# Performance work log

Hardware: AMD Instinct MI355X
Metric: run time of the kernel (lower is better)

## Reference

```python
import jax, jax.numpy as jnp
import numpy as np

B, T, C = 4, 2048, 1024
H = 16
D = C // H  # head_dim = 64

def setup_inputs() -> dict:
    key = jax.random.key(0)
    ks = jax.random.split(key, 5)
    scale = 0.02
    x = jax.random.normal(ks[0], (B, T, C), dtype=jnp.float32)
    # weights stored [in, out] (transpose of torch Linear layout; same math)
    Wqkv = jax.random.normal(ks[1], (C, 3 * C), dtype=jnp.float32) * scale
    bqkv = jnp.zeros((3 * C,), dtype=jnp.float32)
    Wproj = jax.random.normal(ks[2], (C, C), dtype=jnp.float32) * scale
    bproj = jnp.zeros((C,), dtype=jnp.float32)
    return {"x": x, "Wqkv": Wqkv, "bqkv": bqkv, "Wproj": Wproj, "bproj": bproj}

def reference(x, Wqkv, bqkv, Wproj, bproj):
    Bx, Tx, Cx = x.shape
    qkv = x @ Wqkv + bqkv                      # [B,T,3C]
    q, k, v = jnp.split(qkv, 3, axis=2)
    # [B,T,C] -> [B,H,T,D]
    q = q.reshape(Bx, Tx, H, D).transpose(0, 2, 1, 3)
    k = k.reshape(Bx, Tx, H, D).transpose(0, 2, 1, 3)
    v = v.reshape(Bx, Tx, H, D).transpose(0, 2, 1, 3)
    att = jnp.einsum('bhqd,bhkd->bhqk', q, k) / jnp.sqrt(jnp.float32(D))
    causal = jnp.tril(jnp.ones((Tx, Tx), dtype=bool))
    att = jnp.where(causal, att, jnp.float32(-jnp.inf))
    att = jax.nn.softmax(att, axis=-1)
    y = jnp.einsum('bhqk,bhkd->bhqd', att, v)  # [B,H,T,D]
    y = y.transpose(0, 2, 1, 3).reshape(Bx, Tx, Cx)
    return y @ Wproj + bproj
```

## Files before the change

### kernel.cpp

```cpp
#include <hip/hip_runtime.h>
#include <math.h>

#define Bb 4
#define Tt 2048
#define Cc 1024
#define Hh 16
#define Dd 64
#define QSC 0.18033688011112042f

typedef unsigned short ushort_t;
typedef __attribute__((ext_vector_type(8))) short short8;
typedef __attribute__((ext_vector_type(4))) float floatx4;

typedef unsigned int __attribute__((address_space(1))) u32_as1;
typedef unsigned int __attribute__((address_space(3))) u32_as3;

__device__ __forceinline__ void gld_lds16(const void* g, const void* lds_uniform) {
    __builtin_amdgcn_global_load_lds(
        (const u32_as1*)(unsigned long long)g,
        (u32_as3*)(unsigned int)(unsigned long long)lds_uniform,
        16, 0, 0);
}

__device__ inline ushort_t f2bf(float x) {
    unsigned int u = __float_as_uint(x);
    return (ushort_t)((u + 0x7FFFu + ((u >> 16) & 1u)) >> 16);
}

__device__ __forceinline__ void bar() {
    asm volatile("" ::: "memory");
    __builtin_amdgcn_s_barrier();
    asm volatile("" ::: "memory");
}

__global__ __launch_bounds__(256) void convert_kernel(
    const float* __restrict__ in, ushort_t* __restrict__ out, int n4)
{
    int i = blockIdx.x * 256 + threadIdx.x;
    if (i < n4) {
        float4 v = *(const float4*)&in[i * 4];
        ushort_t o[4] = {f2bf(v.x), f2bf(v.y), f2bf(v.z), f2bf(v.w)};
        *(uint2*)&out[i * 4] = *(uint2*)o;
    }
}

__global__ __launch_bounds__(256) void transpose_kernel(
    const float* __restrict__ W, ushort_t* __restrict__ Wt, int K, int N)
{
    __shared__ ushort_t Ts[16][72];
    const int n0 = blockIdx.x * 64;
    const int k0 = blockIdx.y * 16;
    const int t = threadIdx.x;
#pragma unroll
    for (int i = 0; i < 4; i++) {
        int e = t + i * 256;
        int kl = e >> 6, nl = e & 63;
        Ts[kl][nl] = f2bf(W[(size_t)(k0 + kl) * N + n0 + nl]);
    }
    __syncthreads();
    {
        int nl = t >> 2, kl4 = (t & 3) * 4;
        ushort_t o[4] = {Ts[kl4][nl], Ts[kl4 + 1][nl], Ts[kl4 + 2][nl], Ts[kl4 + 3][nl]};
        *(uint2*)&Wt[(size_t)(n0 + nl) * K + k0 + kl4] = *(uint2*)o;
    }
}

template <bool OUT_BF16, bool SCALE_Q>
__global__ __launch_bounds__(512) void gemm256_kernel(
    const ushort_t* __restrict__ A, const ushort_t* __restrict__ Bt,
    const float* __restrict__ bias, void* __restrict__ Co,
    int M, int N, int K)
{
    __shared__ __align__(16) ushort_t Ls[65536];

    const int tid = threadIdx.x;
    const int lane = tid & 63;
    const int w = tid >> 6;
    const int wm = w >> 2, wn = w & 3;
    const int l = lane & 15, q = lane >> 4;
    const int NT = K >> 6;

    const int n0 = blockIdx.x * 256;
    const int m0 = blockIdx.y * 256;

    const int ln = lane ^ (((lane >> 5) & 1) << 1);
    const ushort_t* Ag = A  + (size_t)(m0 + w * 16 + (ln >> 2)) * K + (ln & 3) * 8;
    const ushort_t* Bg = Bt + (size_t)(n0 + w * 16 + (ln >> 2)) * K + (ln & 3) * 8;

    const int swz = l * 32 + ((q * 8) ^ (((l >> 3) & 1) << 4));

    floatx4 acc[2][2][4][2];
#pragma unroll
    for (int qm = 0; qm < 2; qm++)
#pragma unroll
        for (int qn = 0; qn < 2; qn++)
#pragma unroll
            for (int mf = 0; mf < 4; mf++)
#pragma unroll
                for (int nf = 0; nf < 2; nf++)
                    acc[qm][qn][mf][nf] = (floatx4){0.f, 0.f, 0.f, 0.f};

    short8 af[4][2], bf0[2][2], bf1[2][2];

#define STAGE_(SLOT, MAT, HALF, T, GB) {                                        \
    const ushort_t* _g = (GB) + (size_t)(HALF) * 128 * K + (size_t)(T) * 64;    \
    const ushort_t* _l = &Ls[(SLOT) * 32768 + (MAT) * 16384 + (HALF) * 8192 + w * 1024]; \
    gld_lds16(_g, _l);                                                          \
    gld_lds16(_g + 32, _l + 512); }
#define STAGE_A(SLOT, HALF, T) STAGE_((SLOT), 0, (HALF), (T), Ag)
#define STAGE_B(SLOT, HALF, T) STAGE_((SLOT), 1, (HALF), (T), Bg)

#define LDA(SLOT, QM) {                                                         \
    _Pragma("unroll") for (int mf = 0; mf < 4; mf++)                            \
    _Pragma("unroll") for (int kc = 0; kc < 2; kc++)                            \
        af[mf][kc] = *(const short8*)&Ls[(SLOT) * 32768 + (QM) * 8192 +         \
            ((wm * 4 + mf) * 2 + kc) * 512 + swz]; }

#define LDB(SLOT, QN, DST) {                                                    \
    _Pragma("unroll") for (int nf = 0; nf < 2; nf++)                            \
    _Pragma("unroll") for (int kc = 0; kc < 2; kc++)                            \
        DST[nf][kc] = *(const short8*)&Ls[(SLOT) * 32768 + 16384 + (QN) * 8192 + \
            ((wn * 2 + nf) * 2 + kc) * 512 + swz]; }

#define MM(QM, QN, BF) {                                                        \
    __builtin_amdgcn_s_setprio(1);                                              \
    _Pragma("unroll") for (int kc = 0; kc < 2; kc++)                            \
    _Pragma("unroll") for (int mf = 0; mf < 4; mf++)                            \
    _Pragma("unroll") for (int nf = 0; nf < 2; nf++)                            \
        acc[QM][QN][mf][nf] = __builtin_amdgcn_mfma_f32_16x16x32_bf16(          \
            af[mf][kc], BF[nf][kc], acc[QM][QN][mf][nf], 0, 0, 0);              \
    __builtin_amdgcn_s_setprio(0); }

#define LGKM0() asm volatile("s_waitcnt lgkmcnt(0)" ::: "memory")

    STAGE_A(0, 0, 0); STAGE_B(0, 0, 0); STAGE_B(0, 1, 0); STAGE_A(0, 1, 0);
    if (NT > 1) {
        STAGE_A(1, 0, 1); STAGE_B(1, 0, 1); STAGE_B(1, 1, 1);
        asm volatile("s_waitcnt vmcnt(6)" ::: "memory");
    } else {
        asm volatile("s_waitcnt vmcnt(0)" ::: "memory");
    }
    bar();

    for (int g = 0; g < NT; ++g) {
        const int slot = g & 1;

        LDA(slot, 0);
        LDB(slot, 0, bf0);
        if (g + 1 < NT) STAGE_A(slot ^ 1, 1, g + 1);
        bar();
        LGKM0();
        MM(0, 0, bf0);
        bar();

        LDB(slot, 1, bf1);
        if (g + 2 < NT) STAGE_A(slot, 0, g + 2);
        bar();
        LGKM0();
        MM(0, 1, bf1);
        bar();

        LDA(slot, 1);
        if (g + 2 < NT) STAGE_B(slot, 0, g + 2);
        bar();
        LGKM0();
        MM(1, 1, bf1);
        bar();

        if (g + 2 < NT) STAGE_B(slot, 1, g + 2);
        bar();
        LGKM0();
        MM(1, 0, bf0);
        if (g + 1 < NT) {
            if (g + 2 < NT) asm volatile("s_waitcnt vmcnt(6)" ::: "memory");
            else            asm volatile("s_waitcnt vmcnt(0)" ::: "memory");
            bar();
        }
    }

#pragma unroll
    for (int qn = 0; qn < 2; qn++)
#pragma unroll
        for (int nf = 0; nf < 2; nf++) {
            const int col = n0 + qn * 128 + wn * 32 + nf * 16 + l;
            const float bi = bias[col];
            const float sc = (SCALE_Q && col < 1024) ? QSC : 1.0f;
#pragma unroll
            for (int qm = 0; qm < 2; qm++)
#pragma unroll
                for (int mf = 0; mf < 4; mf++)
#pragma unroll
                    for (int r = 0; r < 4; r++) {
                        const int row = m0 + qm * 128 + wm * 64 + mf * 16 + q * 4 + r;
                        const float v = (acc[qm][qn][mf][nf][r] + bi) * sc;
                        if (OUT_BF16)
                            ((ushort_t*)Co)[(size_t)row * N + col] = f2bf(v);
                        else
                            ((float*)Co)[(size_t)row * N + col] = v;
                    }
        }
#undef STAGE_
#undef STAGE_A
#undef STAGE_B
#undef LDA
#undef LDB
#undef MM
#undef LGKM0
}

__device__ __forceinline__ int ks_swz(int I) {
    return I ^ (((I >> 8) & 1) * 0x28) ^ (((I >> 9) & 1) * 0x10);
}
__device__ __forceinline__ int vt_idx(int row, int col) {
    return row * 80 + (col ^ ((((row >> 2) ^ (row >> 4)) & 3) << 3));
}
__device__ __forceinline__ int ps_idx(int row, int col) {
    return row * 80 + (col ^ (((row >> 2) & 3) << 3));
}

__global__ __launch_bounds__(256, 2) void attn_mfma_kernel(
    const ushort_t* __restrict__ qkv, ushort_t* __restrict__ yatt)
{
    __shared__ __align__(16) ushort_t Ks[8 * 512];
    __shared__ __align__(16) ushort_t Vt[80 * 80];
    __shared__ __align__(16) ushort_t Ps[4][16 * 80];

    const int tid = threadIdx.x;
    const int lane = tid & 63;
    const int w = tid >> 6;
    const int quad = lane >> 4;
    const int l = lane & 15;

    const int bh = blockIdx.x;
    const int j = 15 - (int)blockIdx.y;
    const int q0 = j * 128;
    const int b = bh >> 4;
    const int h = bh & 15;
    const size_t base = (size_t)b * Tt * (3 * Cc);
    const int qoff = h * 64;
    const int koff = Cc + h * 64;
    const int voff = 2 * Cc + h * 64;

    for (int i = tid; i < 16 * 64; i += 256)
        Vt[vt_idx(64 + i / 64, i % 64)] = 0x3F80;

    short8 Qf[2][2];
#pragma unroll
    for (int mt = 0; mt < 2; mt++)
#pragma unroll
        for (int kc = 0; kc < 2; kc++)
            Qf[mt][kc] = *(const short8*)&qkv[base
                + (size_t)(q0 + mt * 64 + w * 16 + l) * (3 * Cc)
                + qoff + kc * 32 + quad * 8];

    floatx4 Oacc[2][4];
    floatx4 Lacc[2];
#pragma unroll
    for (int mt = 0; mt < 2; mt++) {
        Lacc[mt] = (floatx4){0.f, 0.f, 0.f, 0.f};
#pragma unroll
        for (int dt = 0; dt < 4; dt++)
            Oacc[mt][dt] = (floatx4){0.f, 0.f, 0.f, 0.f};
    }

    const int srow = tid >> 2;
    const int sd0 = (tid & 3) * 16;
    const int knt = srow >> 4, kl = srow & 15;
    const int kc_s = sd0 >> 5;
    const int qp0 = (sd0 & 31) >> 3;
    const int pcol = (srow & 15) * 4 + (srow >> 4);

    const int ntil = 2 * j + 2;

    const ushort_t* kp0 = &qkv[base + (size_t)srow * (3 * Cc) + koff + sd0];
    const ushort_t* vp0 = &qkv[base + (size_t)srow * (3 * Cc) + voff + sd0];

    uint4 pk0 = *(const uint4*)kp0;
    uint4 pk1 = *(const uint4*)(kp0 + 8);
    uint4 pv0 = *(const uint4*)vp0;
    uint4 pv1 = *(const uint4*)(vp0 + 8);

    const int ksw0 = ks_swz((knt * 2 + kc_s) * 512 + (qp0 * 16 + kl) * 8);
    const int ksw1 = ks_swz((knt * 2 + kc_s) * 512 + ((qp0 + 1) * 16 + kl) * 8);

    for (int kt = 0; kt < ntil; kt++) {
        const int kbase = kt * 64;
        __syncthreads();
        *(uint4*)&Ks[ksw0] = pk0;
        *(uint4*)&Ks[ksw1] = pk1;
        {
            ushort_t tv[16];
            *(uint4*)&tv[0] = pv0;
            *(uint4*)&tv[8] = pv1;
#pragma unroll
            for (int t2 = 0; t2 < 16; t2++) Vt[vt_idx(sd0 + t2, pcol)] = tv[t2];
        }
        __syncthreads();

        if (kt + 1 < ntil) {
            const size_t off = (size_t)(kbase + 64) * (3 * Cc);
            pk0 = *(const uint4*)(kp0 + off);
            pk1 = *(const uint4*)(kp0 + off + 8);
            pv0 = *(const uint4*)(vp0 + off);
            pv1 = *(const uint4*)(vp0 + off + 8);
        }

        short8 Vf[5][2];
#pragma unroll
        for (int dt = 0; dt < 5; dt++)
#pragma unroll
            for (int kc = 0; kc < 2; kc++)
                Vf[dt][kc] = *(const short8*)&Vt[vt_idx(dt * 16 + l, kc * 32 + quad * 8)];

#pragma unroll
        for (int mt = 0; mt < 2; mt++) {
            const int qmin = q0 + mt * 64 + (w << 4);
            if (kbase > qmin + 15) continue;

            floatx4 S[4];
#pragma unroll
            for (int nt = 0; nt < 4; nt++) S[nt] = (floatx4){0.f, 0.f, 0.f, 0.f};
            __builtin_amdgcn_s_setprio(1);
#pragma unroll
            for (int kc = 0; kc < 2; kc++) {
#pragma unroll
                for (int nt = 0; nt < 4; nt++) {
                    short8 kf = *(const short8*)&Ks[ks_swz((nt * 2 + kc) * 512 + lane * 8)];
                    S[nt] = __builtin_amdgcn_mfma_f32_16x16x32_bf16(
                        Qf[mt][kc], kf, S[nt], 0, 0, 0);
                }
            }
            __builtin_amdgcn_s_setprio(0);

            const bool need_mask = (kbase + 63 > qmin);

#pragma unroll
            for (int r = 0; r < 4; r++) {
                const int qrow = qmin + quad * 4 + r;
                float e[4];
#pragma unroll
                for (int nt = 0; nt < 4; nt++) {
                    float s = S[nt][r];
                    if (need_mask && (kbase + nt * 16 + l > qrow)) s = -INFINITY;
                    e[nt] = __builtin_amdgcn_exp2f(s);
                }
                unsigned int u0 = __builtin_amdgcn_perm(
                    __float_as_uint(e[1]), __float_as_uint(e[0]), 0x07060302u);
                unsigned int u1 = __builtin_amdgcn_perm(
                    __float_as_uint(e[3]), __float_as_uint(e[2]), 0x07060302u);
                uint2 pk; pk.x = u0; pk.y = u1;
                *(uint2*)&Ps[w][ps_idx(quad * 4 + r, l * 4)] = pk;
            }
            asm volatile("" ::: "memory");

            short8 Pa0 = *(const short8*)&Ps[w][ps_idx(l, quad * 8)];
            short8 Pa1 = *(const short8*)&Ps[w][ps_idx(l, 32 + quad * 8)];
            __builtin_amdgcn_s_setprio(1);
#pragma unroll
            for (int dt = 0; dt < 4; dt++) {
                Oacc[mt][dt] = __builtin_amdgcn_mfma_f32_16x16x32_bf16(
                    Pa0, Vf[dt][0], Oacc[mt][dt], 0, 0, 0);
                Oacc[mt][dt] = __builtin_amdgcn_mfma_f32_16x16x32_bf16(
                    Pa1, Vf[dt][1], Oacc[mt][dt], 0, 0, 0);
            }
            Lacc[mt] = __builtin_amdgcn_mfma_f32_16x16x32_bf16(
                Pa0, Vf[4][0], Lacc[mt], 0, 0, 0);
            Lacc[mt] = __builtin_amdgcn_mfma_f32_16x16x32_bf16(
                Pa1, Vf[4][1], Lacc[mt], 0, 0, 0);
            __builtin_amdgcn_s_setprio(0);
            asm volatile("" ::: "memory");
        }
    }

#pragma unroll
    for (int mt = 0; mt < 2; mt++)
#pragma unroll
        for (int r = 0; r < 4; r++) {
            const float rl = 1.f / Lacc[mt][r];
            const int qrow = q0 + mt * 64 + (w << 4) + quad * 4 + r;
#pragma unroll
            for (int dt = 0; dt < 4; dt++)
                yatt[(size_t)(b * Tt + qrow) * Cc + h * 64 + dt * 16 + l] =
                    f2bf(Oacc[mt][dt][r] * rl);
        }
}

extern "C" void kernel_launch(void* const* d_in, const int* in_sizes, int n_in,
                              void* d_out, int out_size, void* d_ws, size_t ws_size,
                              hipStream_t stream) {
    const float* x     = (const float*)d_in[0];
    const float* Wqkv  = (const float*)d_in[1];
    const float* bqkv  = (const float*)d_in[2];
    const float* Wproj = (const float*)d_in[3];
    const float* bproj = (const float*)d_in[4];
    float* out = (float*)d_out;

    ushort_t* qkvb   = (ushort_t*)d_ws;
    ushort_t* yattb  = qkvb + (size_t)8192 * 3072;
    ushort_t* xb     = yattb + (size_t)8192 * 1024;
    ushort_t* wqkvt  = xb + (size_t)8192 * 1024;
    ushort_t* wprojt = wqkvt + (size_t)3072 * 1024;

    convert_kernel<<<(8192 * 1024 / 4 + 255) / 256, 256, 0, stream>>>(x, xb, 8192 * 1024 / 4);
    transpose_kernel<<<dim3(3072 / 64, 1024 / 16), 256, 0, stream>>>(Wqkv, wqkvt, 1024, 3072);
    transpose_kernel<<<dim3(1024 / 64, 1024 / 16), 256, 0, stream>>>(Wproj, wprojt, 1024, 1024);

    gemm256_kernel<true, true><<<dim3(3072 / 256, 8192 / 256), 512, 0, stream>>>(
        xb, wqkvt, bqkv, qkvb, 8192, 3072, 1024);
    attn_mfma_kernel<<<dim3(64, 16), 256, 0, stream>>>(qkvb, yattb);
    gemm256_kernel<false, false><<<dim3(1024 / 256, 8192 / 256), 512, 0, stream>>>(
        yattb, wprojt, bproj, out, 8192, 1024, 1024);
}
```

Measured before the change: 270.6 us.

## Split causal attention KV range into chunks with a separate combine kernel

Each query tile's key range is now split into chunks of up to 8 KV tiles, giving 40 work items per (batch, head) instead of 16. Partial unnormalized outputs and row sums go to fp32 workspace, and a new combine kernel sums them, normalizes and writes bf16. The aim is better load balance and more parallelism for the long causal tiles. The cost is extra fp32 traffic for the partials, one more kernel launch, and extra workspace. The partials are summed without max rescaling, which matches the existing unrescaled-exp scheme.

```diff
diff --git a/kernel.cpp b/kernel.cpp
--- a/kernel.cpp
+++ b/kernel.cpp
@@ -219,7 +219,8 @@
 }
 
 __global__ __launch_bounds__(256, 2) void attn_mfma_kernel(
-    const ushort_t* __restrict__ qkv, ushort_t* __restrict__ yatt)
+    const ushort_t* __restrict__ qkv, float* __restrict__ O_part,
+    float* __restrict__ l_part)
 {
     __shared__ __align__(16) ushort_t Ks[8 * 512];
     __shared__ __align__(16) ushort_t Vt[80 * 80];
@@ -232,8 +233,14 @@
     const int l = lane & 15;
 
     const int bh = blockIdx.x;
-    const int j = 15 - (int)blockIdx.y;
+    const int s = 39 - (int)blockIdx.y;
+    int j = 0, ofs = 0;
+    while (ofs + ((j >> 2) + 1) <= s) { ofs += (j >> 2) + 1; ++j; }
+    const int c = s - ofs;
     const int q0 = j * 128;
+    const int kt0 = c * 8;
+    const int kt1 = min(c * 8 + 8, 2 * j + 2);
+
     const int b = bh >> 4;
     const int h = bh & 15;
     const size_t base = (size_t)b * Tt * (3 * Cc);
@@ -270,20 +277,22 @@
     const int qp0 = (sd0 & 31) >> 3;
     const int pcol = (srow & 15) * 4 + (srow >> 4);
 
-    const int ntil = 2 * j + 2;
-
     const ushort_t* kp0 = &qkv[base + (size_t)srow * (3 * Cc) + koff + sd0];
     const ushort_t* vp0 = &qkv[base + (size_t)srow * (3 * Cc) + voff + sd0];
 
-    uint4 pk0 = *(const uint4*)kp0;
-    uint4 pk1 = *(const uint4*)(kp0 + 8);
-    uint4 pv0 = *(const uint4*)vp0;
-    uint4 pv1 = *(const uint4*)(vp0 + 8);
+    {
+        const size_t off0 = (size_t)(kt0 * 64) * (3 * Cc);
+        (void)off0;
+    }
+    uint4 pk0 = *(const uint4*)(kp0 + (size_t)(kt0 * 64) * (3 * Cc));
+    uint4 pk1 = *(const uint4*)(kp0 + (size_t)(kt0 * 64) * (3 * Cc) + 8);
+    uint4 pv0 = *(const uint4*)(vp0 + (size_t)(kt0 * 64) * (3 * Cc));
+    uint4 pv1 = *(const uint4*)(vp0 + (size_t)(kt0 * 64) * (3 * Cc) + 8);
 
     const int ksw0 = ks_swz((knt * 2 + kc_s) * 512 + (qp0 * 16 + kl) * 8);
     const int ksw1 = ks_swz((knt * 2 + kc_s) * 512 + ((qp0 + 1) * 16 + kl) * 8);
 
-    for (int kt = 0; kt < ntil; kt++) {
+    for (int kt = kt0; kt < kt1; kt++) {
         const int kbase = kt * 64;
         __syncthreads();
         *(uint4*)&Ks[ksw0] = pk0;
@@ -297,8 +306,8 @@
         }
         __syncthreads();
 
-        if (kt + 1 < ntil) {
-            const size_t off = (size_t)(kbase + 64) * (3 * Cc);
+        if (kt + 1 < kt1) {
+            const size_t off = (size_t)((kt + 1) * 64) * (3 * Cc);
             pk0 = *(const uint4*)(kp0 + off);
             pk1 = *(const uint4*)(kp0 + off + 8);
             pv0 = *(const uint4*)(vp0 + off);
@@ -340,9 +349,9 @@
                 float e[4];
 #pragma unroll
                 for (int nt = 0; nt < 4; nt++) {
-                    float s = S[nt][r];
-                    if (need_mask && (kbase + nt * 16 + l > qrow)) s = -INFINITY;
-                    e[nt] = __builtin_amdgcn_exp2f(s);
+                    float s2 = S[nt][r];
+                    if (need_mask && (kbase + nt * 16 + l > qrow)) s2 = -INFINITY;
+                    e[nt] = __builtin_amdgcn_exp2f(s2);
                 }
                 unsigned int u0 = __builtin_amdgcn_perm(
                     __float_as_uint(e[1]), __float_as_uint(e[0]), 0x07060302u);
@@ -372,17 +381,56 @@
         }
     }
 
+    const int slot = bh * 40 + s;
+    const size_t obase = (size_t)slot * 8192;
 #pragma unroll
     for (int mt = 0; mt < 2; mt++)
 #pragma unroll
         for (int r = 0; r < 4; r++) {
-            const float rl = 1.f / Lacc[mt][r];
-            const int qrow = q0 + mt * 64 + (w << 4) + quad * 4 + r;
+            const int row = mt * 64 + (w << 4) + quad * 4 + r;
+            if (l == 0) l_part[(size_t)slot * 128 + row] = Lacc[mt][r];
 #pragma unroll
             for (int dt = 0; dt < 4; dt++)
-                yatt[(size_t)(b * Tt + qrow) * Cc + h * 64 + dt * 16 + l] =
-                    f2bf(Oacc[mt][dt][r] * rl);
-        }
+                O_part[obase + (size_t)row * 64 + dt * 16 + l] = Oacc[mt][dt][r];
+        }
+}
+
+__global__ __launch_bounds__(256) void attn_combine_kernel(
+    const float* __restrict__ O_part, const float* __restrict__ l_part,
+    ushort_t* __restrict__ yatt)
+{
+    const int bh = blockIdx.x;
+    const int j  = blockIdx.y;
+    const int b = bh >> 4, h = bh & 15;
+    const int qd = j >> 2, rd = j & 3;
+    const int off = j + 2 * qd * (qd - 1) + rd * qd;
+    const int nc = qd + 1;
+    const int slot0 = bh * 40 + off;
+
+    __shared__ float ls[128];
+    const int t = threadIdx.x;
+    if (t < 128) {
+        float sum = 0.f;
+        for (int cc = 0; cc < nc; ++cc)
+            sum += l_part[(size_t)(slot0 + cc) * 128 + t];
+        ls[t] = 1.f / sum;
+    }
+    __syncthreads();
+
+    for (int e = t; e < 2048; e += 256) {
+        const int row = e >> 4;
+        float4 acc = ((const float4*)(O_part + (size_t)slot0 * 8192))[e];
+        for (int cc = 1; cc < nc; ++cc) {
+            float4 v = ((const float4*)(O_part + (size_t)(slot0 + cc) * 8192))[e];
+            acc.x += v.x; acc.y += v.y; acc.z += v.z; acc.w += v.w;
+        }
+        const float rl = ls[row];
+        ushort_t o[4] = {f2bf(acc.x * rl), f2bf(acc.y * rl),
+                         f2bf(acc.z * rl), f2bf(acc.w * rl)};
+        const int qrow = j * 128 + row;
+        const int col = (e & 15) * 4;
+        *(uint2*)&yatt[(size_t)(b * Tt + qrow) * Cc + h * 64 + col] = *(uint2*)o;
+    }
 }
 
 extern "C" void kernel_launch(void* const* d_in, const int* in_sizes, int n_in,
@@ -400,6 +448,8 @@
     ushort_t* xb     = yattb + (size_t)8192 * 1024;
     ushort_t* wqkvt  = xb + (size_t)8192 * 1024;
     ushort_t* wprojt = wqkvt + (size_t)3072 * 1024;
+    float* opart     = (float*)(wprojt + (size_t)1024 * 1024);
+    float* lpart     = opart + (size_t)2560 * 8192;
 
     convert_kernel<<<(8192 * 1024 / 4 + 255) / 256, 256, 0, stream>>>(x, xb, 8192 * 1024 / 4);
     transpose_kernel<<<dim3(3072 / 64, 1024 / 16), 256, 0, stream>>>(Wqkv, wqkvt, 1024, 3072);
@@ -407,7 +457,8 @@
 
     gemm256_kernel<true, true><<<dim3(3072 / 256, 8192 / 256), 512, 0, stream>>>(
         xb, wqkvt, bqkv, qkvb, 8192, 3072, 1024);
-    attn_mfma_kernel<<<dim3(64, 16), 256, 0, stream>>>(qkvb, yattb);
+    attn_mfma_kernel<<<dim3(64, 40), 256, 0, stream>>>(qkvb, opart, lpart);
+    attn_combine_kernel<<<dim3(64, 16), 256, 0, stream>>>(opart, lpart, yattb);
     gemm256_kernel<false, false><<<dim3(1024 / 256, 8192 / 256), 512, 0, stream>>>(
         yattb, wprojt, bproj, out, 8192, 1024, 1024);
 }
```

Measured after the change: 300.1 us. +10.9%, slower.

## Double-buffer K/V tiles in LDS to drop one barrier per iteration

Applied to the files above, without the earlier changes.

Attention kernel now keeps two LDS slots for K and transposed V. The next tile is written into the other slot while the current one is being computed, and the global prefetch moves two tiles ahead. This leaves one __syncthreads per iteration instead of two and overlaps the LDS stores with the MFMA work. The cost is more LDS per block (about 38 KB), which could limit occupancy at 2 blocks per CU, and the extra register pressure from the prefetch.

```diff
diff --git a/kernel.cpp b/kernel.cpp
--- a/kernel.cpp
+++ b/kernel.cpp
@@ -218,11 +218,14 @@
     return row * 80 + (col ^ (((row >> 2) & 3) << 3));
 }
 
+#define KS_SLOT 4096
+#define VT_SLOT 6400
+
 __global__ __launch_bounds__(256, 2) void attn_mfma_kernel(
     const ushort_t* __restrict__ qkv, ushort_t* __restrict__ yatt)
 {
-    __shared__ __align__(16) ushort_t Ks[8 * 512];
-    __shared__ __align__(16) ushort_t Vt[80 * 80];
+    __shared__ __align__(16) ushort_t Ks[2 * KS_SLOT];
+    __shared__ __align__(16) ushort_t Vt[2 * VT_SLOT];
     __shared__ __align__(16) ushort_t Ps[4][16 * 80];
 
     const int tid = threadIdx.x;
@@ -241,8 +244,11 @@
     const int koff = Cc + h * 64;
     const int voff = 2 * Cc + h * 64;
 
-    for (int i = tid; i < 16 * 64; i += 256)
-        Vt[vt_idx(64 + i / 64, i % 64)] = 0x3F80;
+    for (int i = tid; i < 16 * 64; i += 256) {
+        const int vi = vt_idx(64 + i / 64, i % 64);
+        Vt[vi] = 0x3F80;
+        Vt[VT_SLOT + vi] = 0x3F80;
+    }
 
     short8 Qf[2][2];
 #pragma unroll
@@ -275,42 +281,50 @@
     const ushort_t* kp0 = &qkv[base + (size_t)srow * (3 * Cc) + koff + sd0];
     const ushort_t* vp0 = &qkv[base + (size_t)srow * (3 * Cc) + voff + sd0];
 
+    const int ksw0 = ks_swz((knt * 2 + kc_s) * 512 + (qp0 * 16 + kl) * 8);
+    const int ksw1 = ks_swz((knt * 2 + kc_s) * 512 + ((qp0 + 1) * 16 + kl) * 8);
+
     uint4 pk0 = *(const uint4*)kp0;
     uint4 pk1 = *(const uint4*)(kp0 + 8);
     uint4 pv0 = *(const uint4*)vp0;
     uint4 pv1 = *(const uint4*)(vp0 + 8);
 
-    const int ksw0 = ks_swz((knt * 2 + kc_s) * 512 + (qp0 * 16 + kl) * 8);
-    const int ksw1 = ks_swz((knt * 2 + kc_s) * 512 + ((qp0 + 1) * 16 + kl) * 8);
+#define WRITE_TILE(SLOT) {                                                      \
+    *(uint4*)&Ks[(SLOT) * KS_SLOT + ksw0] = pk0;                                \
+    *(uint4*)&Ks[(SLOT) * KS_SLOT + ksw1] = pk1;                                \
+    ushort_t tv[16];                                                            \
+    *(uint4*)&tv[0] = pv0;                                                      \
+    *(uint4*)&tv[8] = pv1;                                                      \
+    _Pragma("unroll") for (int t2 = 0; t2 < 16; t2++)                           \
+        Vt[(SLOT) * VT_SLOT + vt_idx(sd0 + t2, pcol)] = tv[t2]; }
+
+#define LOAD_TILE(KT) {                                                         \
+    const size_t _off = (size_t)((KT) * 64) * (3 * Cc);                         \
+    pk0 = *(const uint4*)(kp0 + _off);                                          \
+    pk1 = *(const uint4*)(kp0 + _off + 8);                                      \
+    pv0 = *(const uint4*)(vp0 + _off);                                          \
+    pv1 = *(const uint4*)(vp0 + _off + 8); }
+
+    WRITE_TILE(0);
+    if (ntil > 1) LOAD_TILE(1);
+    __syncthreads();
 
     for (int kt = 0; kt < ntil; kt++) {
         const int kbase = kt * 64;
-        __syncthreads();
-        *(uint4*)&Ks[ksw0] = pk0;
-        *(uint4*)&Ks[ksw1] = pk1;
-        {
-            ushort_t tv[16];
-            *(uint4*)&tv[0] = pv0;
-            *(uint4*)&tv[8] = pv1;
-#pragma unroll
-            for (int t2 = 0; t2 < 16; t2++) Vt[vt_idx(sd0 + t2, pcol)] = tv[t2];
+        const int slot = kt & 1;
+
+        short8 Vf[5][2];
+#pragma unroll
+        for (int dt = 0; dt < 5; dt++)
+#pragma unroll
+            for (int kc = 0; kc < 2; kc++)
+                Vf[dt][kc] = *(const short8*)&Vt[slot * VT_SLOT
+                    + vt_idx(dt * 16 + l, kc * 32 + quad * 8)];
+
+        if (kt + 1 < ntil) {
+            WRITE_TILE(slot ^ 1);
+            if (kt + 2 < ntil) LOAD_TILE(kt + 2);
         }
-        __syncthreads();
-
-        if (kt + 1 < ntil) {
-            const size_t off = (size_t)(kbase + 64) * (3 * Cc);
-            pk0 = *(const uint4*)(kp0 + off);
-            pk1 = *(const uint4*)(kp0 + off + 8);
-            pv0 = *(const uint4*)(vp0 + off);
-            pv1 = *(const uint4*)(vp0 + off + 8);
-        }
-
-        short8 Vf[5][2];
-#pragma unroll
-        for (int dt = 0; dt < 5; dt++)
-#pragma unroll
-            for (int kc = 0; kc < 2; kc++)
-                Vf[dt][kc] = *(const short8*)&Vt[vt_idx(dt * 16 + l, kc * 32 + quad * 8)];
 
 #pragma unroll
         for (int mt = 0; mt < 2; mt++) {
@@ -325,7 +339,8 @@
             for (int kc = 0; kc < 2; kc++) {
 #pragma unroll
                 for (int nt = 0; nt < 4; nt++) {
-                    short8 kf = *(const short8*)&Ks[ks_swz((nt * 2 + kc) * 512 + lane * 8)];
+                    short8 kf = *(const short8*)&Ks[slot * KS_SLOT
+                        + ks_swz((nt * 2 + kc) * 512 + lane * 8)];
                     S[nt] = __builtin_amdgcn_mfma_f32_16x16x32_bf16(
                         Qf[mt][kc], kf, S[nt], 0, 0, 0);
                 }
@@ -340,9 +355,9 @@
                 float e[4];
 #pragma unroll
                 for (int nt = 0; nt < 4; nt++) {
-                    float s = S[nt][r];
-                    if (need_mask && (kbase + nt * 16 + l > qrow)) s = -INFINITY;
-                    e[nt] = __builtin_amdgcn_exp2f(s);
+                    float s2 = S[nt][r];
+                    if (need_mask && (kbase + nt * 16 + l > qrow)) s2 = -INFINITY;
+                    e[nt] = __builtin_amdgcn_exp2f(s2);
                 }
                 unsigned int u0 = __builtin_amdgcn_perm(
                     __float_as_uint(e[1]), __float_as_uint(e[0]), 0x07060302u);
@@ -370,6 +385,8 @@
             __builtin_amdgcn_s_setprio(0);
             asm volatile("" ::: "memory");
         }
+
+        __syncthreads();
     }
 
 #pragma unroll
@@ -383,6 +400,8 @@
                 yatt[(size_t)(b * Tt + qrow) * Cc + h * 64 + dt * 16 + l] =
                     f2bf(Oacc[mt][dt][r] * rl);
         }
+#undef WRITE_TILE
+#undef LOAD_TILE
 }
 
 extern "C" void kernel_launch(void* const* d_in, const int* in_sizes, int n_in,
```

Measured after the change: 269.6 us. No clear change (-0.4%).
